# Kernel optimization log

Hardware: AMD Instinct MI355X
Metric: run time of the kernel (lower is better)

The kernel has to match this reference:

```python
import jax, jax.numpy as jnp
import numpy as np

# static config (must match init_kwargs)
B, HIS, N, DIN = 16, 13, 400, 16
HID, S, PRED, LAYERS = 256, 4, 12, 3
NG = S * N  # nodes in the combined virtual graph
DEG = 8     # avg out-degree of base adjacency
EPS = 1e-5


def _build_graph():
    """Reproduce _combine_graph (offset bug included) + edge weights."""
    rng = np.random.default_rng(0)
    cols = np.argsort(rng.random((N, N)), axis=1)[:, :DEG]  # [N, DEG] distinct cols per row
    w = rng.uniform(0.1, 1.0, size=(N, DEG)).astype(np.float32)
    rows = np.repeat(np.arange(N), DEG)
    c = cols.ravel()
    off = (S - 1) * N
    # first block rows: [adj | adj]; last diagonal block: adj
    src = np.concatenate([rows, rows, rows + off]).astype(np.int32)
    dst = np.concatenate([c, c + N, c + off]).astype(np.int32)
    ew = np.concatenate([w.ravel(), w.ravel(), w.ravel()]).astype(np.float32)
    return src, dst, ew


def _checkpoints():
    mark, chp = S, []
    while mark < HIS:
        chp.append(mark)
        mark += S - 1
    if chp[-1] != HIS:
        chp.append(HIS)
    return chp


def setup_inputs() -> dict:
    key = jax.random.key(0)
    ks = jax.random.split(key, 9)
    src, dst, ew = _build_graph()
    sc = 0.05
    return {
        "inputs": jax.random.normal(ks[0], (B, HIS, N, DIN), jnp.float32),
        "W_in": jax.random.normal(ks[1], (DIN, HID), jnp.float32) * sc,
        "b_in": jax.random.normal(ks[2], (HID,), jnp.float32) * sc,
        "gcn_W": jax.random.normal(ks[3], (LAYERS, HID, HID), jnp.float32) * sc,
        "gcn_b": jax.random.normal(ks[4], (LAYERS, HID), jnp.float32) * sc,
        "W1": jax.random.normal(ks[5], (1, PRED), jnp.float32) * sc,
        "b1": jax.random.normal(ks[6], (PRED,), jnp.float32) * sc,
        "W2": jax.random.normal(ks[7], (HID, 1), jnp.float32) * sc,
        "b2": jax.random.normal(ks[8], (1,), jnp.float32) * sc,
        "edge_w": jnp.asarray(ew),
        "src": jnp.asarray(src),
        "dst": jnp.asarray(dst),
    }


def _gcn(h, src, dst, edge_w, inv_out, inv_in, gcn_W, gcn_b):
    """LAYERS-deep GraphConv (norm='both', edge weights), ReLU between layers.
    h: [B, NG, HID]. Dropout is identity (eval)."""
    seg = jax.vmap(lambda m: jax.ops.segment_sum(m, dst, num_segments=NG))
    for i in range(LAYERS):
        hs = h * inv_out[None, :, None]          # D_out^{-1/2} on src side
        msg = hs[:, src, :] * edge_w[None, :, None]  # [B, E, HID]
        agg = seg(msg) * inv_in[None, :, None]   # D_in^{-1/2} on dst side
        h_new = agg @ gcn_W[i] + gcn_b[i]
        h = jax.nn.relu(h_new) if i < LAYERS - 1 else h_new
    return h


def reference(inputs, W_in, b_in, gcn_W, gcn_b, W1, b1, W2, b2, edge_w, src, dst):
    # unweighted degrees for symmetric normalization (guard isolated nodes)
    ones = jnp.ones_like(edge_w)
    out_deg = jnp.zeros((NG,), jnp.float32).at[src].add(ones)
    in_deg = jnp.zeros((NG,), jnp.float32).at[dst].add(ones)
    inv_out = jax.lax.rsqrt(jnp.maximum(out_deg, 1.0))
    inv_in = jax.lax.rsqrt(jnp.maximum(in_deg, 1.0))

    x = inputs @ W_in + b_in  # [B, HIS, N, HID]
    last = None
    left = 0
    for idx, right in enumerate(_checkpoints()):
        if idx == 0:
            fs = x[:, left:right]                       # [B, S, N, HID]
        else:
            fs = jnp.concatenate([last, x[:, left:right]], axis=1)
        h = fs.reshape(B, NG, HID)
        res = h
        h = _gcn(h, src, dst, edge_w, inv_out, inv_in, gcn_W, gcn_b) + res
        # nn.LayerNorm([B*S*N, HID], elementwise_affine=False) on a tensor of
        # exactly that shape => normalize over ALL elements jointly
        h = (h - h.mean()) * jax.lax.rsqrt(h.var() + EPS)
        h = h.reshape(B, S, N, HID)
        last = h[:, -1:, :, :]  # [B, 1, N, HID]
        left = right

    t = jnp.transpose(last, (0, 3, 2, 1))   # [B, HID, N, 1]
    o = t @ W1 + b1                          # [B, HID, N, PRED]
    o = jnp.transpose(o, (0, 3, 2, 1))       # [B, PRED, N, HID]
    o = jax.nn.relu(o)
    return o @ W2 + b2                       # [B, PRED, N, 1]
```

## Files before the change

### kernel.cpp

```cpp
#include <hip/hip_runtime.h>

#define BB 16
#define HIS 13
#define NN 400
#define DIN 16
#define HID 256
#define PRED 12
#define NE 9600
#define EPSF 1e-5f
#define HSZ ((size_t)25600*256)
#define BAND ((size_t)NN*BB*HID)
#define ROWS_BAND (NN*BB)
#define CSR_CAP 6144

typedef __attribute__((ext_vector_type(8))) short short8v;
typedef __attribute__((ext_vector_type(4))) float f32x4;

__device__ __forceinline__ short f2bf(float x) {
    unsigned u = __float_as_uint(x);
    return (short)((u + 0x7FFF + ((u >> 16) & 1)) >> 16);
}
__device__ __forceinline__ float bf2f(short x) {
    return __uint_as_float(((unsigned)(unsigned short)x) << 16);
}
__device__ __forceinline__ void gload16(const void* g, void* l) {
    __builtin_amdgcn_global_load_lds((const __attribute__((address_space(1))) void*)g,
                                     (__attribute__((address_space(3))) void*)l,
                                     16, 0, 0);
}

__global__ __launch_bounds__(256) void k_prep(
    const int* __restrict__ src, const int* __restrict__ dst,
    const float* __restrict__ ew, const float* __restrict__ gcn_W,
    const float* __restrict__ inp, const float* __restrict__ W_in,
    const float* __restrict__ b_in, const float* __restrict__ gb2,
    float* __restrict__ inv_in, float* __restrict__ csum,
    int* __restrict__ csr_off, int* __restrict__ csr_src,
    float* __restrict__ cf1, float* __restrict__ cf2,
    short* __restrict__ Wt, short* __restrict__ xproj,
    float* __restrict__ stats)
{
    __shared__ __align__(16) char SM[17408];
    int t = threadIdx.x, bi = blockIdx.x;
    if (bi == 0) {
        int* ideg  = (int*)SM;
        int* cnt   = ideg + 400;
        int* offl  = cnt + 400;
        int* scan_t = offl + 401;
        float* csuml = (float*)(scan_t + 256);
        for (int g = t; g < 400; g += 256) { ideg[g] = 0; cnt[g] = 0; csuml[g] = 0.f; }
        if (t == 9) stats[9] = (1.0f - EPSF) * (float)HSZ;
        __syncthreads();
        for (int e = t; e < 3200; e += 256) atomicAdd(&ideg[dst[e]], 1);
        __syncthreads();
        int s = 0, p0 = 0, p1 = 0;
        if (t < 200) {
            p0 = (ideg[2 * t] + 7) & ~7;
            p1 = (ideg[2 * t + 1] + 7) & ~7;
            s = p0 + p1;
        }
        scan_t[t] = s;
        __syncthreads();
        for (int o = 1; o < 256; o <<= 1) {
            int v = (t >= o) ? scan_t[t - o] : 0;
            __syncthreads();
            scan_t[t] += v;
            __syncthreads();
        }
        if (t < 200) { int base = scan_t[t] - s; offl[2 * t] = base; offl[2 * t + 1] = base + p0; }
        if (t == 255) offl[400] = scan_t[255];
        __syncthreads();
        int cap = offl[400];
        for (int g = t; g < 401; g += 256) csr_off[g] = offl[g];
        for (int g = t; g < 400; g += 256) inv_in[g] = rsqrtf(fmaxf((float)ideg[g], 1.f));
        for (int i = t; i < cap; i += 256) { csr_src[i] = 0; cf1[i] = 0.f; cf2[i] = 0.f; }
        __syncthreads();
        float rs16 = rsqrtf(16.0f), rs8 = rsqrtf(8.0f);
        for (int e = t; e < 3200; e += 256) {
            int d = dst[e];
            int r = e >> 3;
            int p = offl[d] + atomicAdd(&cnt[d], 1);
            float w = ew[e];
            float c1 = w * rs16;
            csr_src[p] = r;
            cf1[p] = c1;
            cf2[p] = w * rs8;
            atomicAdd(&csuml[d], c1);
        }
        __syncthreads();
        for (int g = t; g < 400; g += 256) csum[g] = csuml[g];
    } else if (bi <= 48) {
        float (*S)[65] = (float(*)[65])SM;
        int tile = bi - 1;
        int l = tile / 16, sub = tile % 16;
        int k0 = (sub >> 2) * 64, n0 = (sub & 3) * 64;
        int tr = t >> 6, tc = t & 63;
#pragma unroll
        for (int i = 0; i < 16; ++i) {
            int r = i * 4 + tr;
            S[r][tc] = gcn_W[(size_t)l * 65536 + (size_t)(k0 + r) * 256 + n0 + tc];
        }
        __syncthreads();
#pragma unroll
        for (int i = 0; i < 16; ++i) {
            int n = i * 4 + tr;
            Wt[(size_t)l * 65536 + (size_t)(n0 + n) * 256 + k0 + tc] = f2bf(S[tc][n]);
        }
    } else {
        float* rbuf = (float*)SM;
        float wr[16];
#pragma unroll
        for (int d = 0; d < 16; ++d) wr[d] = W_in[d * 256 + t];
        float bvv = b_in[t];
        int job0 = (bi - 49) * 4;
        int time = job0 / 400;
        int n0 = job0 % 400;
        bool isStat = (time == 2 || time == 5 || time == 8 || time == 11);
        float gb = isStat ? gb2[t] : 0.f;
        float s1 = 0.f, s2 = 0.f;
        for (int j = 0; j < 4; ++j) {
            int n = n0 + j;
            float acc[16];
#pragma unroll
            for (int b = 0; b < 16; ++b) acc[b] = bvv;
#pragma unroll
            for (int b = 0; b < 16; ++b) {
                const float* xr = inp + (((size_t)b * HIS + time) * NN + n) * DIN;
#pragma unroll
                for (int d = 0; d < 16; ++d) acc[b] = fmaf(xr[d], wr[d], acc[b]);
            }
            if (isStat) {
#pragma unroll
                for (int b = 0; b < 16; ++b) {
                    float v = acc[b] + gb;
                    s1 += v; s2 += v * v;
                }
            } else {
                size_t gbase = (size_t)time * BAND + ((size_t)n * 16) * 256 + t;
#pragma unroll
                for (int b = 0; b < 16; ++b) xproj[gbase + (size_t)b * 256] = f2bf(acc[b]);
            }
        }
        if (isStat) {
#pragma unroll
            for (int o = 32; o > 0; o >>= 1) {
                s1 += __shfl_down(s1, o, 64);
                s2 += __shfl_down(s2, o, 64);
            }
            int wid = t >> 6, lane = t & 63;
            if (lane == 0) { rbuf[wid] = s1; rbuf[4 + wid] = s2; }
            __syncthreads();
            if (t == 0) {
                int it = (time - 2) / 3;
                atomicAdd(&stats[it * 2],     rbuf[0] + rbuf[1] + rbuf[2] + rbuf[3]);
                atomicAdd(&stats[it * 2 + 1], rbuf[4] + rbuf[5] + rbuf[6] + rbuf[7]);
            }
        }
    }
}

template <int MODE>
__global__ __launch_bounds__(256) void k_layer(
    const short* __restrict__ hX, const short* __restrict__ hY,
    const float* __restrict__ stA, const float* __restrict__ csum,
    const float* __restrict__ inv_in, const int* __restrict__ csr_off,
    const int* __restrict__ csr_src, const float* __restrict__ cf1,
    const float* __restrict__ cf2,
    const short* __restrict__ Bt, const float* __restrict__ bias,
    const short* __restrict__ resX0, const float* __restrict__ stR,
    const short* __restrict__ resX1, const short* __restrict__ resY,
    short* __restrict__ C, float* __restrict__ stats)
{
    __shared__ short As[32][264];
    __shared__ short Bs[2][8192];
    __shared__ float red[512];
    int tid = threadIdx.x;
    int wid = tid >> 6, l = tid & 63;
    int l15 = l & 15, l4 = l >> 4;
    int blk = blockIdx.x;
    int isY = blk >= 200;
    int gl = (isY ? blk - 200 : blk) * 2;
    int rowL0 = gl * 16;
    int wn = wid * 64;
    const short* hsrc = isY ? hY : hX;
    const float* cf = isY ? cf2 : cf1;

    float am = 1.f, moff = 0.f;
    if (MODE == 0 && !isY) {
        float mean = stA[0] * (1.f / (float)HSZ);
        float var  = stA[1] * (1.f / (float)HSZ) - mean * mean;
        float istd = rsqrtf(var + EPSF);
        am = istd; moff = mean * istd;
    }
    int br = l >> 2;
    int kd = (l & 3) ^ ((br >> 1) & 3);
    for (int ch = wid; ch < 16; ch += 4)
        gload16(Bt + ((size_t)(ch * 16 + br)) * 256 + kd * 8, &Bs[0][ch * 512]);

    {
        int b = tid >> 4, hsc = (tid & 15) * 16;
        const size_t lane_off = (size_t)b * HID + hsc;
        for (int gi = 0; gi < 2; ++gi) {
            int g = gl + gi;
            int beg = csr_off[g], end = csr_off[g + 1];
            float acc[16];
#pragma unroll
            for (int i = 0; i < 16; ++i) acc[i] = 0.f;
            for (int j = beg; j < end; j += 8) {
                int ss[8]; float cc[8];
#pragma unroll
                for (int u = 0; u < 8; ++u) { ss[u] = csr_src[j + u]; cc[u] = cf[j + u]; }
                short8v va[8], vb[8];
#pragma unroll
                for (int u = 0; u < 8; ++u) {
                    const short8v* q = (const short8v*)&hsrc[(size_t)ss[u] * 4096 + lane_off];
                    va[u] = q[0]; vb[u] = q[1];
                }
#pragma unroll
                for (int u = 0; u < 8; ++u) {
#pragma unroll
                    for (int i = 0; i < 8; ++i) {
                        acc[i]     = fmaf(cc[u], bf2f(va[u][i]), acc[i]);
                        acc[8 + i] = fmaf(cc[u], bf2f(vb[u][i]), acc[8 + i]);
                    }
                }
            }
            float s = inv_in[g];
            float addv = (MODE == 0 && !isY) ? (-moff * csum[g]) : 0.f;
            short8v o0, o1;
#pragma unroll
            for (int i = 0; i < 8; ++i) o0[i] = f2bf(s * fmaf(am, acc[i], addv));
#pragma unroll
            for (int i = 0; i < 8; ++i) o1[i] = f2bf(s * fmaf(am, acc[8 + i], addv));
            int row = gi * 16 + b;
            *(short8v*)&As[row][hsc]     = o0;
            *(short8v*)&As[row][hsc + 8] = o1;
        }
    }
    __syncthreads();

    f32x4 cacc[2][4] = {};
    int xsw = (l4 ^ ((l15 >> 1) & 3)) * 8;
    for (int kc = 0; kc < 8; ++kc) {
        int cur = kc & 1;
        if (kc < 7) {
            int k0n = (kc + 1) * 32;
            for (int ch = wid; ch < 16; ch += 4)
                gload16(Bt + ((size_t)(ch * 16 + br)) * 256 + k0n + kd * 8,
                        &Bs[cur ^ 1][ch * 512]);
        }
        int k0 = kc * 32;
        short8v av[2], bv[4];
#pragma unroll
        for (int mi = 0; mi < 2; ++mi)
            av[mi] = *(const short8v*)&As[mi * 16 + l15][k0 + l4 * 8];
#pragma unroll
        for (int ni = 0; ni < 4; ++ni)
            bv[ni] = *(const short8v*)&Bs[cur][(wn + ni * 16 + l15) * 32 + xsw];
#pragma unroll
        for (int mi = 0; mi < 2; ++mi)
#pragma unroll
            for (int ni = 0; ni < 4; ++ni)
                cacc[mi][ni] = __builtin_amdgcn_mfma_f32_16x16x32_bf16(
                    av[mi], bv[ni], cacc[mi][ni], 0, 0, 0);
        __syncthreads();
    }

    if (MODE <= 1) {
#pragma unroll
        for (int ni = 0; ni < 4; ++ni) {
            int col = wn + ni * 16 + l15;
            float bvv = bias[col];
#pragma unroll
            for (int mi = 0; mi < 2; ++mi) {
#pragma unroll
                for (int r = 0; r < 4; ++r) {
                    float v = fmaxf(cacc[mi][ni][r] + bvv, 0.f);
                    As[mi * 16 + l4 * 4 + r][col] = f2bf(v);
                }
            }
        }
        __syncthreads();
        int row = tid >> 3, cs = (tid & 7) * 32;
        size_t gb = ((size_t)(isY ? ROWS_BAND : 0) + rowL0 + row) * HID + cs;
#pragma unroll
        for (int i = 0; i < 4; ++i)
            *(short8v*)&C[gb + i * 8] = *(const short8v*)&As[row][cs + i * 8];
    } else {
        float s1 = 0.f, s2 = 0.f;
        if (!isY) {
            float meanR = stR[0] * (1.f / (float)HSZ);
            float varR  = stR[1] * (1.f / (float)HSZ) - meanR * meanR;
            float istdR = rsqrtf(varR + EPSF);
#pragma unroll
            for (int ni = 0; ni < 4; ++ni) {
                int col = wn + ni * 16 + l15;
                float bvv = bias[col];
#pragma unroll
                for (int mi = 0; mi < 2; ++mi) {
#pragma unroll
                    for (int r = 0; r < 4; ++r) {
                        int rowg = rowL0 + mi * 16 + l4 * 4 + r;
                        size_t ix = (size_t)rowg * HID + col;
                        float base = cacc[mi][ni][r] + bvv;
                        float v1 = base + (bf2f(resX0[ix]) - meanR) * istdR;
                        float v2 = base + bf2f(resX1[ix]);
                        s1 += v1 + v2;
                        s2 += v1 * v1 + v2 * v2;
                    }
                }
            }
        } else {
#pragma unroll
            for (int ni = 0; ni < 4; ++ni) {
                int col = wn + ni * 16 + l15;
                float bvv = bias[col];
#pragma unroll
                for (int mi = 0; mi < 2; ++mi) {
#pragma unroll
                    for (int r = 0; r < 4; ++r) {
                        int rowl = mi * 16 + l4 * 4 + r;
                        size_t ix = (size_t)(rowL0 + rowl) * HID + col;
                        float v = cacc[mi][ni][r] + bvv + bf2f(resY[ix]);
                        s1 += v; s2 += v * v;
                        As[rowl][col] = f2bf(v);
                    }
                }
            }
            __syncthreads();
            int row = tid >> 3, cs = (tid & 7) * 32;
            size_t gb = (size_t)(rowL0 + row) * HID + cs;
#pragma unroll
            for (int i = 0; i < 4; ++i)
                *(short8v*)&C[gb + i * 8] = *(const short8v*)&As[row][cs + i * 8];
        }
        red[tid] = s1; red[256 + tid] = s2;
        __syncthreads();
        for (int o = 128; o > 0; o >>= 1) {
            if (tid < o) { red[tid] += red[tid + o]; red[256 + tid] += red[256 + tid + o]; }
            __syncthreads();
        }
        if (tid == 0) { atomicAdd(&stats[0], red[0]); atomicAdd(&stats[1], red[256]); }
    }
}

__global__ void k_head(const short* __restrict__ hlast, const float* __restrict__ st,
                       const float* __restrict__ W1, const float* __restrict__ b1,
                       const float* __restrict__ W2, const float* __restrict__ b2,
                       float* __restrict__ out) {
    float mean = st[0] * (1.0f / (float)HSZ);
    float var  = st[1] * (1.0f / (float)HSZ) - mean * mean;
    float istd = rsqrtf(var + EPSF);
    int n = blockIdx.x, b = blockIdx.y, tid = threadIdx.x;
    float v  = (bf2f(hlast[((size_t)n * BB + b) * HID + tid]) - mean) * istd;
    float w2 = W2[tid];
    float b2v = b2[0];
    __shared__ float ps[4];
    for (int p = 0; p < PRED; ++p) {
        float t = fmaxf(fmaf(v, W1[p], b1[p]), 0.f) * w2;
#pragma unroll
        for (int o = 32; o > 0; o >>= 1) t += __shfl_down(t, o, 64);
        int wid = tid >> 6, lane = tid & 63;
        if (lane == 0) ps[wid] = t;
        __syncthreads();
        if (tid == 0) out[(size_t)(b * PRED + p) * NN + n] = ps[0] + ps[1] + ps[2] + ps[3] + b2v;
        __syncthreads();
    }
}

extern "C" void kernel_launch(void* const* d_in, const int* in_sizes, int n_in,
                              void* d_out, int out_size, void* d_ws, size_t ws_size,
                              hipStream_t stream) {
    const float* inp   = (const float*)d_in[0];
    const float* W_in  = (const float*)d_in[1];
    const float* b_in  = (const float*)d_in[2];
    const float* gcn_W = (const float*)d_in[3];
    const float* gcn_b = (const float*)d_in[4];
    const float* W1    = (const float*)d_in[5];
    const float* b1    = (const float*)d_in[6];
    const float* W2    = (const float*)d_in[7];
    const float* b2    = (const float*)d_in[8];
    const float* ew    = (const float*)d_in[9];
    const int*   src   = (const int*)d_in[10];
    const int*   dst   = (const int*)d_in[11];
    float* out = (float*)d_out;

    char* w = (char*)d_ws;
    auto alloc = [&](size_t bytes) {
        char* p = w;
        w += (bytes + 255) & ~(size_t)255;
        return p;
    };
    short* hA    = (short*)alloc((size_t)2 * ROWS_BAND * HID * 2);
    short* hB    = (short*)alloc((size_t)2 * ROWS_BAND * HID * 2);
    short* hl0   = (short*)alloc(BAND * 2);
    short* hl1   = (short*)alloc(BAND * 2);
    short* xproj = (short*)alloc((size_t)13 * BAND * 2);
    short* Wt    = (short*)alloc((size_t)3 * 65536 * 2);
    float* inv_in  = (float*)alloc(400 * 4);
    float* csum    = (float*)alloc(400 * 4);
    int*   csr_off = (int*)alloc(401 * 4);
    int*   csr_srcv= (int*)alloc(CSR_CAP * 4);
    float* cf1     = (float*)alloc(CSR_CAP * 4);
    float* cf2     = (float*)alloc(CSR_CAP * 4);
    float* stats   = (float*)alloc(12 * 4);

    hipMemsetAsync(stats, 0, 12 * 4, stream);
    k_prep<<<1349, 256, 0, stream>>>(src, dst, ew, gcn_W, inp, W_in, b_in,
                                     gcn_b + 512, inv_in, csum, csr_off,
                                     csr_srcv, cf1, cf2, Wt, xproj, stats);

    const int lefts[4] = {0, 4, 7, 10};
    const size_t RB = (size_t)ROWS_BAND * HID;
    for (int it = 0; it < 4; ++it) {
        int t1 = (it == 0) ? 1 : lefts[it];
        int t3 = (it == 0) ? 3 : lefts[it] + 2;
        const short* hlp = (it == 0) ? xproj : ((it & 1) ? hl0 : hl1);
        const float* stA = (it == 0) ? stats + 8 : stats + (it - 1) * 2;
        short* cur = (it & 1) ? hl1 : hl0;
        k_layer<0><<<400, 256, 0, stream>>>(hlp, xproj + (size_t)t3 * BAND, stA, csum,
                                            inv_in, csr_off, csr_srcv, cf1, cf2,
                                            Wt, gcn_b,
                                            nullptr, nullptr, nullptr, nullptr,
                                            hA, nullptr);
        k_layer<1><<<400, 256, 0, stream>>>(hA, hA + RB, stats + 8, csum,
                                            inv_in, csr_off, csr_srcv, cf1, cf2,
                                            Wt + 65536, gcn_b + 256,
                                            nullptr, nullptr, nullptr, nullptr,
                                            hB, nullptr);
        k_layer<2><<<400, 256, 0, stream>>>(hB, hB + RB, stats + 8, csum,
                                            inv_in, csr_off, csr_srcv, cf1, cf2,
                                            Wt + 131072, gcn_b + 512,
                                            hlp, stA, xproj + (size_t)t1 * BAND,
                                            xproj + (size_t)t3 * BAND,
                                            cur, stats + it * 2);
    }

    k_head<<<dim3(NN, BB), 256, 0, stream>>>(hl1, stats + 6, W1, b1, W2, b2, out);
}
```

Before: 284.2 us.

## Load GEMM weight fragments directly into registers instead of LDS double-buffer

```diff
diff --git a/kernel.cpp b/kernel.cpp
--- a/kernel.cpp
+++ b/kernel.cpp
@@ -22,11 +22,6 @@
 }
 __device__ __forceinline__ float bf2f(short x) {
     return __uint_as_float(((unsigned)(unsigned short)x) << 16);
-}
-__device__ __forceinline__ void gload16(const void* g, void* l) {
-    __builtin_amdgcn_global_load_lds((const __attribute__((address_space(1))) void*)g,
-                                     (__attribute__((address_space(3))) void*)l,
-                                     16, 0, 0);
 }
 
 __global__ __launch_bounds__(256) void k_prep(
@@ -172,7 +167,6 @@
     short* __restrict__ C, float* __restrict__ stats)
 {
     __shared__ short As[32][264];
-    __shared__ short Bs[2][8192];
     __shared__ float red[512];
     int tid = threadIdx.x;
     int wid = tid >> 6, l = tid & 63;
@@ -192,10 +186,6 @@
         float istd = rsqrtf(var + EPSF);
         am = istd; moff = mean * istd;
     }
-    int br = l >> 2;
-    int kd = (l & 3) ^ ((br >> 1) & 3);
-    for (int ch = wid; ch < 16; ch += 4)
-        gload16(Bt + ((size_t)(ch * 16 + br)) * 256 + kd * 8, &Bs[0][ch * 512]);
 
     {
         int b = tid >> 4, hsc = (tid & 15) * 16;
@@ -237,34 +227,32 @@
             *(short8v*)&As[row][hsc + 8] = o1;
         }
     }
+
+    short8v breg[4][8];
+#pragma unroll
+    for (int ni = 0; ni < 4; ++ni)
+#pragma unroll
+        for (int kc = 0; kc < 8; ++kc)
+            breg[ni][kc] = *(const short8v*)
+                &Bt[(size_t)(wn + ni * 16 + l15) * 256 + kc * 32 + l4 * 8];
+
     __syncthreads();
 
     f32x4 cacc[2][4] = {};
-    int xsw = (l4 ^ ((l15 >> 1) & 3)) * 8;
+#pragma unroll
     for (int kc = 0; kc < 8; ++kc) {
-        int cur = kc & 1;
-        if (kc < 7) {
-            int k0n = (kc + 1) * 32;
-            for (int ch = wid; ch < 16; ch += 4)
-                gload16(Bt + ((size_t)(ch * 16 + br)) * 256 + k0n + kd * 8,
-                        &Bs[cur ^ 1][ch * 512]);
-        }
         int k0 = kc * 32;
-        short8v av[2], bv[4];
-#pragma unroll
-        for (int mi = 0; mi < 2; ++mi)
-            av[mi] = *(const short8v*)&As[mi * 16 + l15][k0 + l4 * 8];
-#pragma unroll
-        for (int ni = 0; ni < 4; ++ni)
-            bv[ni] = *(const short8v*)&Bs[cur][(wn + ni * 16 + l15) * 32 + xsw];
+        short8v av[2];
+        av[0] = *(const short8v*)&As[l15][k0 + l4 * 8];
+        av[1] = *(const short8v*)&As[16 + l15][k0 + l4 * 8];
 #pragma unroll
         for (int mi = 0; mi < 2; ++mi)
 #pragma unroll
             for (int ni = 0; ni < 4; ++ni)
                 cacc[mi][ni] = __builtin_amdgcn_mfma_f32_16x16x32_bf16(
-                    av[mi], bv[ni], cacc[mi][ni], 0, 0, 0);
-        __syncthreads();
-    }
+                    av[mi], breg[ni][kc], cacc[mi][ni], 0, 0, 0);
+    }
+    __syncthreads();
 
     if (MODE <= 1) {
 #pragma unroll
```

Result: slower. 316.8 us (+11.5%).
